# Kernel optimization log

Measured on AMD Instinct MI355X. Metric: run time of the kernel, lower is better.

## Reference

```python
import jax, jax.numpy as jnp
import numpy as np

TEMPERATURE = 0.5


def setup_inputs() -> dict:
    key = jax.random.key(0)
    k1, k2 = jax.random.split(key)
    N, D = 4096, 512
    emb_i = jax.random.normal(k1, (N, D), dtype=jnp.float32)
    emb_j = jax.random.normal(k2, (N, D), dtype=jnp.float32)
    return {"emb_i": emb_i, "emb_j": emb_j}


def reference(emb_i, emb_j):
    # L2-normalize each embedding row (F.normalize, dim=1)
    z_i = emb_i / jnp.linalg.norm(emb_i, axis=1, keepdims=True)
    z_j = emb_j / jnp.linalg.norm(emb_j, axis=1, keepdims=True)
    reps = jnp.concatenate([z_i, z_j], axis=0)  # [2N, D]
    N = emb_i.shape[0]
    M = 2 * N
    # cosine similarity of normalized vectors == dot product -> [2N, 2N]
    sim = jnp.einsum('id,jd->ij', reps, reps) / TEMPERATURE
    # denominator: sum_k!=i exp(sim[i,k]); original multiplies by one-hot complement
    exp_sim = jnp.exp(sim)
    denom = jnp.sum(exp_sim, axis=1) - jnp.diagonal(exp_sim)  # [2N]
    log_denom = jnp.log(denom)
    # positive pairs: (k, k+N) and (k+N, k)
    idx = jnp.arange(N)
    pos_ij = sim[idx, idx + N]          # sim(k, k+N)/T
    pos_ji = sim[idx + N, idx]          # sim(k+N, k)/T
    loss = jnp.sum(-(pos_ij - log_denom[:N]) - (pos_ji - log_denom[N:]))
    return loss / (2.0 * N)
```

## Files before the change

### kernel.cpp

```cpp
#include <hip/hip_runtime.h>
#include <cstdint>
#include <cstddef>

constexpr int N_ROWS = 4096;
constexpr int D      = 512;
constexpr int M      = 8192;
constexpr int NTILE  = 64;
constexpr int NBLK   = NTILE * (NTILE + 1) / 2;
constexpr int BKB    = 128;
constexpr int LDSB   = 128 * BKB;

using f32x4 = __attribute__((ext_vector_type(4))) float;
using i32x4 = __attribute__((ext_vector_type(4))) int;
using i32x8 = __attribute__((ext_vector_type(8))) int;

#define ASYNC_CP16(gsrc, ldst)                                                      \
    __builtin_amdgcn_global_load_lds(                                               \
        (const __attribute__((address_space(1))) unsigned int*)(gsrc),              \
        (__attribute__((address_space(3))) unsigned int*)(ldst), 16, 0, 0)

#define SS_FP8(pk, accum)                                                           \
    do {                                                                            \
        float f0 = __builtin_amdgcn_cvt_f32_fp8((pk), 0);                           \
        float f1 = __builtin_amdgcn_cvt_f32_fp8((pk), 1);                           \
        float f2 = __builtin_amdgcn_cvt_f32_fp8((pk), 2);                           \
        float f3 = __builtin_amdgcn_cvt_f32_fp8((pk), 3);                           \
        (accum) += f0 * f0 + f1 * f1 + f2 * f2 + f3 * f3;                           \
    } while (0)

__global__ __launch_bounds__(256) void normpos_kernel(
    const float* __restrict__ emb_i, const float* __restrict__ emb_j,
    uint8_t* __restrict__ zb, float* __restrict__ diagss,
    float* __restrict__ pos)
{
    const int wave = threadIdx.x >> 6, lane = threadIdx.x & 63;
    const int k = blockIdx.x * 4 + wave;

    const float4* a = (const float4*)(emb_i + (size_t)k * D);
    const float4* b = (const float4*)(emb_j + (size_t)k * D);
    float4 a0 = a[lane * 2], a1 = a[lane * 2 + 1];
    float4 b0 = b[lane * 2], b1 = b[lane * 2 + 1];

    float ssi = a0.x*a0.x + a0.y*a0.y + a0.z*a0.z + a0.w*a0.w
              + a1.x*a1.x + a1.y*a1.y + a1.z*a1.z + a1.w*a1.w;
    float ssj = b0.x*b0.x + b0.y*b0.y + b0.z*b0.z + b0.w*b0.w
              + b1.x*b1.x + b1.y*b1.y + b1.z*b1.z + b1.w*b1.w;
    float dp  = a0.x*b0.x + a0.y*b0.y + a0.z*b0.z + a0.w*b0.w
              + a1.x*b1.x + a1.y*b1.y + a1.z*b1.z + a1.w*b1.w;
    #pragma unroll
    for (int off = 32; off; off >>= 1) {
        ssi += __shfl_xor(ssi, off, 64);
        ssj += __shfl_xor(ssj, off, 64);
        dp  += __shfl_xor(dp,  off, 64);
    }
    const float invi = rsqrtf(ssi), invj = rsqrtf(ssj);

    const float zi[8] = {a0.x*invi, a0.y*invi, a0.z*invi, a0.w*invi,
                         a1.x*invi, a1.y*invi, a1.z*invi, a1.w*invi};
    const float zj[8] = {b0.x*invj, b0.y*invj, b0.z*invj, b0.w*invj,
                         b1.x*invj, b1.y*invj, b1.z*invj, b1.w*invj};

    int pi0 = __builtin_amdgcn_cvt_pk_fp8_f32(zi[0], zi[1], 0, false);
    pi0     = __builtin_amdgcn_cvt_pk_fp8_f32(zi[2], zi[3], pi0, true);
    int pi1 = __builtin_amdgcn_cvt_pk_fp8_f32(zi[4], zi[5], 0, false);
    pi1     = __builtin_amdgcn_cvt_pk_fp8_f32(zi[6], zi[7], pi1, true);
    int pj0 = __builtin_amdgcn_cvt_pk_fp8_f32(zj[0], zj[1], 0, false);
    pj0     = __builtin_amdgcn_cvt_pk_fp8_f32(zj[2], zj[3], pj0, true);
    int pj1 = __builtin_amdgcn_cvt_pk_fp8_f32(zj[4], zj[5], 0, false);
    pj1     = __builtin_amdgcn_cvt_pk_fp8_f32(zj[6], zj[7], pj1, true);

    float dssi = 0.f, dssj = 0.f;
    SS_FP8(pi0, dssi);
    SS_FP8(pi1, dssi);
    SS_FP8(pj0, dssj);
    SS_FP8(pj1, dssj);

    const unsigned long long vi =
        ((unsigned long long)(unsigned)pi1 << 32) | (unsigned)pi0;
    const unsigned long long vj =
        ((unsigned long long)(unsigned)pj1 << 32) | (unsigned)pj0;
    *(unsigned long long*)(zb + (size_t)k * D + lane * 8)            = vi;
    *(unsigned long long*)(zb + (size_t)(k + N_ROWS) * D + lane * 8) = vj;

    #pragma unroll
    for (int off = 32; off; off >>= 1) {
        dssi += __shfl_xor(dssi, off, 64);
        dssj += __shfl_xor(dssj, off, 64);
    }
    if (lane == 0) {
        diagss[k]          = dssi;
        diagss[k + N_ROWS] = dssj;
        pos[k]             = 2.0f * dp * invi * invj;
    }
}

__global__ __launch_bounds__(256, 2) void simgemm_kernel(
    const uint8_t* __restrict__ zb, float* __restrict__ partials)
{
    __shared__ i32x4 AsV[2 * LDSB / 16];
    __shared__ i32x4 BsV[2 * LDSB / 16];
    __shared__ float rp[4][64];
    __shared__ float cp4[4][64];
    uint8_t* As = (uint8_t*)AsV;
    uint8_t* Bs = (uint8_t*)BsV;

    const int tid  = threadIdx.x;
    const int wave = tid >> 6, lane = tid & 63;
    const int l15  = lane & 15, ks = lane >> 4;

    const int t = blockIdx.x;
    int bi = (int)((129.0f - sqrtf(129.0f * 129.0f - 8.0f * (float)t)) * 0.5f);
    while (bi > 0 && bi * (129 - bi) / 2 > t) --bi;
    while ((bi + 1) * (129 - (bi + 1)) / 2 <= t) ++bi;
    const int bj = bi + (t - bi * (129 - bi) / 2);
    const bool diag = (bi == bj);

    const int wrow = (wave >> 1) * 64, wcol = (wave & 1) * 64;

    const int srow = (lane >> 3);
    const int scol = ((lane & 7) ^ ((lane >> 3) & 7)) * 16;
    const uint8_t* gA = zb + (size_t)(bi * 128 + wave * 32 + srow) * D + scol;
    const uint8_t* gB = zb + (size_t)(bj * 128 + wave * 32 + srow) * D + scol;
    uint8_t* lA = As + wave * 32 * BKB;
    uint8_t* lB = Bs + wave * 32 * BKB;

    #pragma unroll
    for (int c = 0; c < 4; ++c) {
        ASYNC_CP16(gA + (size_t)c * 8 * D, lA + c * 8 * BKB);
        ASYNC_CP16(gB + (size_t)c * 8 * D, lB + c * 8 * BKB);
    }

    f32x4 acc[4][4] = {};

    for (int it = 0; it < D / BKB; ++it) {
        __syncthreads();

        if (it + 1 < D / BKB) {
            const int kc  = (it + 1) * BKB;
            const int off = ((it + 1) & 1) * LDSB;
            #pragma unroll
            for (int c = 0; c < 4; ++c) {
                ASYNC_CP16(gA + kc + (size_t)c * 8 * D, lA + off + c * 8 * BKB);
                ASYNC_CP16(gB + kc + (size_t)c * 8 * D, lB + off + c * 8 * BKB);
            }
        }

        const int cb = (it & 1) * LDSB;
        i32x8 af[4], bg[4];
        #pragma unroll
        for (int f = 0; f < 4; ++f) {
            {
                const int R = wrow + f * 16 + l15;
                const uint8_t* base = As + cb + R * BKB;
                const int sw = (R & 7);
                i32x4 lo = *(const i32x4*)(base + ((ks * 2)     ^ sw) * 16);
                i32x4 hi = *(const i32x4*)(base + ((ks * 2 + 1) ^ sw) * 16);
                af[f] = __builtin_shufflevector(lo, hi, 0, 1, 2, 3, 4, 5, 6, 7);
            }
            {
                const int R = wcol + f * 16 + l15;
                const uint8_t* base = Bs + cb + R * BKB;
                const int sw = (R & 7);
                i32x4 lo = *(const i32x4*)(base + ((ks * 2)     ^ sw) * 16);
                i32x4 hi = *(const i32x4*)(base + ((ks * 2 + 1) ^ sw) * 16);
                bg[f] = __builtin_shufflevector(lo, hi, 0, 1, 2, 3, 4, 5, 6, 7);
            }
        }
        #pragma unroll
        for (int i = 0; i < 4; ++i)
            #pragma unroll
            for (int j = 0; j < 4; ++j)
                acc[i][j] = __builtin_amdgcn_mfma_scale_f32_16x16x128_f8f6f4(
                    af[i], bg[j], acc[i][j], 0, 0, 0, 0x7F, 0, 0x7F);
    }

    float rowp[4][4] = {};
    #pragma unroll
    for (int j = 0; j < 4; ++j) {
        float cpj = 0.f;
        #pragma unroll
        for (int i = 0; i < 4; ++i)
            #pragma unroll
            for (int r = 0; r < 4; ++r) {
                float e = __expf(2.0f * acc[i][j][r]);
                rowp[i][r] += e;
                cpj += e;
            }
        if (!diag) {
            cpj += __shfl_xor(cpj, 16, 64);
            cpj += __shfl_xor(cpj, 32, 64);
            if (ks == 0) cp4[wave][j * 16 + l15] = cpj;
        }
    }
    #pragma unroll
    for (int i = 0; i < 4; ++i)
        #pragma unroll
        for (int r = 0; r < 4; ++r) {
            float e = rowp[i][r];
            e += __shfl_xor(e, 1, 64);
            e += __shfl_xor(e, 2, 64);
            e += __shfl_xor(e, 4, 64);
            e += __shfl_xor(e, 8, 64);
            if (l15 == 0) rp[wave][i * 16 + ks * 4 + r] = e;
        }
    __syncthreads();

    float* pA = partials + (size_t)(bi * NTILE + bj) * 128;
    float* pB = partials + (size_t)(bj * NTILE + bi) * 128;
    if (tid < 128) {
        const int h = tid >> 6, rr = tid & 63;
        pA[tid] = rp[h * 2][rr] + rp[h * 2 + 1][rr];
    } else if (!diag) {
        const int c = tid - 128, h = c >> 6, cc = c & 63;
        pB[c] = cp4[h][cc] + cp4[h + 2][cc];
    }
}

__global__ __launch_bounds__(256) void rowfin_kernel(
    const float* __restrict__ partials, const float* __restrict__ diagss,
    const float* __restrict__ pos, float* __restrict__ lgpart)
{
    const int r  = blockIdx.x;
    const int ri = threadIdx.x & 127;
    const int ch = threadIdx.x >> 7;
    const float* base = partials + (size_t)r * NTILE * 128 + ri;
    float s = 0.f;
    #pragma unroll
    for (int c = 0; c < 32; ++c)
        s += base[(size_t)(ch * 32 + c) * 128];
    __shared__ float half1[128];
    __shared__ float red[4];
    if (ch == 1) half1[ri] = s;
    __syncthreads();
    float lg = 0.f;
    if (ch == 0) {
        float rs = s + half1[ri];
        int row = r * 128 + ri;
        lg = __logf(rs - __expf(2.0f * diagss[row]));
    }
    if (threadIdx.x < 64)
        lg -= 2.0f * pos[r * 64 + threadIdx.x];
    #pragma unroll
    for (int off = 32; off; off >>= 1) lg += __shfl_xor(lg, off, 64);
    const int wave = threadIdx.x >> 6, lane = threadIdx.x & 63;
    if (lane == 0) red[wave] = lg;
    __syncthreads();
    if (threadIdx.x == 0) lgpart[r] = red[0] + red[1] + red[2] + red[3];
}

__global__ __launch_bounds__(64) void loss_kernel(
    const float* __restrict__ lgpart, float* __restrict__ out)
{
    float local = lgpart[threadIdx.x];
    #pragma unroll
    for (int off = 32; off; off >>= 1) local += __shfl_xor(local, off, 64);
    if (threadIdx.x == 0) out[0] = local * (1.0f / 8192.0f);
}

extern "C" void kernel_launch(void* const* d_in, const int* in_sizes, int n_in,
                              void* d_out, int out_size, void* d_ws, size_t ws_size,
                              hipStream_t stream)
{
    const float* emb_i = (const float*)d_in[0];
    const float* emb_j = (const float*)d_in[1];

    uint8_t* zb = (uint8_t*)d_ws;
    float* partials = (float*)((char*)d_ws + (size_t)M * D);
    float* diagss   = partials + (size_t)NTILE * NTILE * 128;
    float* pos      = diagss + M;
    float* lgpart   = pos + N_ROWS;
    float* out      = (float*)d_out;

    normpos_kernel<<<N_ROWS / 4, 256, 0, stream>>>(emb_i, emb_j, zb, diagss, pos);
    simgemm_kernel<<<NBLK, 256, 0, stream>>>(zb, partials);
    rowfin_kernel<<<NTILE, 256, 0, stream>>>(partials, diagss, pos, lgpart);
    loss_kernel<<<1, 64, 0, stream>>>(lgpart, out);
}
```

Measured before the change: 110.8 us.

## Drop LDS double buffering to single buffer and raise occupancy to four blocks

Replaces the double-buffered LDS staging with a single buffer per operand. Each K step now loads, synchronises, then computes, with an extra barrier before the next load. This halves LDS use, and launch bounds are raised to allow four blocks per CU so other blocks hide the load latency instead of in-block prefetch. It also hoists the swizzle offsets out of the fragment loop. The cost is lost intra-block overlap, an extra barrier per iteration, and tighter register limits that may cause spills.

```diff
diff --git a/kernel.cpp b/kernel.cpp
--- a/kernel.cpp
+++ b/kernel.cpp
@@ -94,11 +94,11 @@
     }
 }
 
-__global__ __launch_bounds__(256, 2) void simgemm_kernel(
+__global__ __launch_bounds__(256, 4) void simgemm_kernel(
     const uint8_t* __restrict__ zb, float* __restrict__ partials)
 {
-    __shared__ i32x4 AsV[2 * LDSB / 16];
-    __shared__ i32x4 BsV[2 * LDSB / 16];
+    __shared__ i32x4 AsV[LDSB / 16];
+    __shared__ i32x4 BsV[LDSB / 16];
     __shared__ float rp[4][64];
     __shared__ float cp4[4][64];
     uint8_t* As = (uint8_t*)AsV;
@@ -124,45 +124,34 @@
     uint8_t* lA = As + wave * 32 * BKB;
     uint8_t* lB = Bs + wave * 32 * BKB;
 
-    #pragma unroll
-    for (int c = 0; c < 4; ++c) {
-        ASYNC_CP16(gA + (size_t)c * 8 * D, lA + c * 8 * BKB);
-        ASYNC_CP16(gB + (size_t)c * 8 * D, lB + c * 8 * BKB);
-    }
-
     f32x4 acc[4][4] = {};
+    const int sw  = l15 & 7;
+    const int co0 = ((ks * 2)     ^ sw) * 16;
+    const int co1 = ((ks * 2 + 1) ^ sw) * 16;
 
     for (int it = 0; it < D / BKB; ++it) {
+        if (it > 0) __syncthreads();
+        const int kc = it * BKB;
+        #pragma unroll
+        for (int c = 0; c < 4; ++c) {
+            ASYNC_CP16(gA + kc + (size_t)c * 8 * D, lA + c * 8 * BKB);
+            ASYNC_CP16(gB + kc + (size_t)c * 8 * D, lB + c * 8 * BKB);
+        }
         __syncthreads();
 
-        if (it + 1 < D / BKB) {
-            const int kc  = (it + 1) * BKB;
-            const int off = ((it + 1) & 1) * LDSB;
-            #pragma unroll
-            for (int c = 0; c < 4; ++c) {
-                ASYNC_CP16(gA + kc + (size_t)c * 8 * D, lA + off + c * 8 * BKB);
-                ASYNC_CP16(gB + kc + (size_t)c * 8 * D, lB + off + c * 8 * BKB);
-            }
-        }
-
-        const int cb = (it & 1) * LDSB;
         i32x8 af[4], bg[4];
         #pragma unroll
         for (int f = 0; f < 4; ++f) {
             {
-                const int R = wrow + f * 16 + l15;
-                const uint8_t* base = As + cb + R * BKB;
-                const int sw = (R & 7);
-                i32x4 lo = *(const i32x4*)(base + ((ks * 2)     ^ sw) * 16);
-                i32x4 hi = *(const i32x4*)(base + ((ks * 2 + 1) ^ sw) * 16);
+                const uint8_t* base = As + (wrow + f * 16 + l15) * BKB;
+                i32x4 lo = *(const i32x4*)(base + co0);
+                i32x4 hi = *(const i32x4*)(base + co1);
                 af[f] = __builtin_shufflevector(lo, hi, 0, 1, 2, 3, 4, 5, 6, 7);
             }
             {
-                const int R = wcol + f * 16 + l15;
-                const uint8_t* base = Bs + cb + R * BKB;
-                const int sw = (R & 7);
-                i32x4 lo = *(const i32x4*)(base + ((ks * 2)     ^ sw) * 16);
-                i32x4 hi = *(const i32x4*)(base + ((ks * 2 + 1) ^ sw) * 16);
+                const uint8_t* base = Bs + (wcol + f * 16 + l15) * BKB;
+                i32x4 lo = *(const i32x4*)(base + co0);
+                i32x4 hi = *(const i32x4*)(base + co1);
                 bg[f] = __builtin_shufflevector(lo, hi, 0, 1, 2, 3, 4, 5, 6, 7);
             }
         }
```

New measurement: 119.2 us. +7.6%, slower.

## Split GEMM tile across eight waves with 32x64 per-wave subtiles

Applied to the files above, without the earlier changes.

The similarity GEMM block grows from 256 to 512 threads. Each wave now computes a 32x64 subtile instead of 64x64, which halves the accumulator registers and loads per wave. The swizzle offsets are hoisted out of the k-loop, and the row and column partial reductions are reorganised for eight waves. The goal is more waves in flight to hide LDS and MFMA latency, at the cost of more B-fragment LDS traffic per MFMA and a larger cross-wave reduction.

```diff
diff --git a/kernel.cpp b/kernel.cpp
--- a/kernel.cpp
+++ b/kernel.cpp
@@ -94,13 +94,13 @@
     }
 }
 
-__global__ __launch_bounds__(256, 2) void simgemm_kernel(
+__global__ __launch_bounds__(512, 4) void simgemm_kernel(
     const uint8_t* __restrict__ zb, float* __restrict__ partials)
 {
     __shared__ i32x4 AsV[2 * LDSB / 16];
     __shared__ i32x4 BsV[2 * LDSB / 16];
-    __shared__ float rp[4][64];
-    __shared__ float cp4[4][64];
+    __shared__ float rp[8][32];
+    __shared__ float cp8[8][64];
     uint8_t* As = (uint8_t*)AsV;
     uint8_t* Bs = (uint8_t*)BsV;
 
@@ -115,22 +115,25 @@
     const int bj = bi + (t - bi * (129 - bi) / 2);
     const bool diag = (bi == bj);
 
-    const int wrow = (wave >> 1) * 64, wcol = (wave & 1) * 64;
-
-    const int srow = (lane >> 3);
+    const int wrow = (wave >> 1) * 32;
+    const int wcol = (wave & 1) * 64;
+
     const int scol = ((lane & 7) ^ ((lane >> 3) & 7)) * 16;
-    const uint8_t* gA = zb + (size_t)(bi * 128 + wave * 32 + srow) * D + scol;
-    const uint8_t* gB = zb + (size_t)(bj * 128 + wave * 32 + srow) * D + scol;
-    uint8_t* lA = As + wave * 32 * BKB;
-    uint8_t* lB = Bs + wave * 32 * BKB;
-
-    #pragma unroll
-    for (int c = 0; c < 4; ++c) {
+    const uint8_t* gA = zb + (size_t)(bi * 128 + wave * 16 + (lane >> 3)) * D + scol;
+    const uint8_t* gB = zb + (size_t)(bj * 128 + wave * 16 + (lane >> 3)) * D + scol;
+    uint8_t* lA = As + wave * 16 * BKB;
+    uint8_t* lB = Bs + wave * 16 * BKB;
+
+    #pragma unroll
+    for (int c = 0; c < 2; ++c) {
         ASYNC_CP16(gA + (size_t)c * 8 * D, lA + c * 8 * BKB);
         ASYNC_CP16(gB + (size_t)c * 8 * D, lB + c * 8 * BKB);
     }
 
-    f32x4 acc[4][4] = {};
+    f32x4 acc[2][4] = {};
+    const int sw  = l15 & 7;
+    const int co0 = ((ks * 2)     ^ sw) * 16;
+    const int co1 = ((ks * 2 + 1) ^ sw) * 16;
 
     for (int it = 0; it < D / BKB; ++it) {
         __syncthreads();
@@ -139,47 +142,42 @@
             const int kc  = (it + 1) * BKB;
             const int off = ((it + 1) & 1) * LDSB;
             #pragma unroll
-            for (int c = 0; c < 4; ++c) {
+            for (int c = 0; c < 2; ++c) {
                 ASYNC_CP16(gA + kc + (size_t)c * 8 * D, lA + off + c * 8 * BKB);
                 ASYNC_CP16(gB + kc + (size_t)c * 8 * D, lB + off + c * 8 * BKB);
             }
         }
 
         const int cb = (it & 1) * LDSB;
-        i32x8 af[4], bg[4];
+        i32x8 af[2], bg[4];
+        #pragma unroll
+        for (int f = 0; f < 2; ++f) {
+            const uint8_t* base = As + cb + (wrow + f * 16 + l15) * BKB;
+            i32x4 lo = *(const i32x4*)(base + co0);
+            i32x4 hi = *(const i32x4*)(base + co1);
+            af[f] = __builtin_shufflevector(lo, hi, 0, 1, 2, 3, 4, 5, 6, 7);
+        }
         #pragma unroll
         for (int f = 0; f < 4; ++f) {
-            {
-                const int R = wrow + f * 16 + l15;
-                const uint8_t* base = As + cb + R * BKB;
-                const int sw = (R & 7);
-                i32x4 lo = *(const i32x4*)(base + ((ks * 2)     ^ sw) * 16);
-                i32x4 hi = *(const i32x4*)(base + ((ks * 2 + 1) ^ sw) * 16);
-                af[f] = __builtin_shufflevector(lo, hi, 0, 1, 2, 3, 4, 5, 6, 7);
-            }
-            {
-                const int R = wcol + f * 16 + l15;
-                const uint8_t* base = Bs + cb + R * BKB;
-                const int sw = (R & 7);
-                i32x4 lo = *(const i32x4*)(base + ((ks * 2)     ^ sw) * 16);
-                i32x4 hi = *(const i32x4*)(base + ((ks * 2 + 1) ^ sw) * 16);
-                bg[f] = __builtin_shufflevector(lo, hi, 0, 1, 2, 3, 4, 5, 6, 7);
-            }
-        }
-        #pragma unroll
-        for (int i = 0; i < 4; ++i)
+            const uint8_t* base = Bs + cb + (wcol + f * 16 + l15) * BKB;
+            i32x4 lo = *(const i32x4*)(base + co0);
+            i32x4 hi = *(const i32x4*)(base + co1);
+            bg[f] = __builtin_shufflevector(lo, hi, 0, 1, 2, 3, 4, 5, 6, 7);
+        }
+        #pragma unroll
+        for (int i = 0; i < 2; ++i)
             #pragma unroll
             for (int j = 0; j < 4; ++j)
                 acc[i][j] = __builtin_amdgcn_mfma_scale_f32_16x16x128_f8f6f4(
                     af[i], bg[j], acc[i][j], 0, 0, 0, 0x7F, 0, 0x7F);
     }
 
-    float rowp[4][4] = {};
+    float rowp[2][4] = {};
     #pragma unroll
     for (int j = 0; j < 4; ++j) {
         float cpj = 0.f;
         #pragma unroll
-        for (int i = 0; i < 4; ++i)
+        for (int i = 0; i < 2; ++i)
             #pragma unroll
             for (int r = 0; r < 4; ++r) {
                 float e = __expf(2.0f * acc[i][j][r]);
@@ -189,11 +187,11 @@
         if (!diag) {
             cpj += __shfl_xor(cpj, 16, 64);
             cpj += __shfl_xor(cpj, 32, 64);
-            if (ks == 0) cp4[wave][j * 16 + l15] = cpj;
-        }
-    }
-    #pragma unroll
-    for (int i = 0; i < 4; ++i)
+            if (ks == 0) cp8[wave][j * 16 + l15] = cpj;
+        }
+    }
+    #pragma unroll
+    for (int i = 0; i < 2; ++i)
         #pragma unroll
         for (int r = 0; r < 4; ++r) {
             float e = rowp[i][r];
@@ -208,11 +206,11 @@
     float* pA = partials + (size_t)(bi * NTILE + bj) * 128;
     float* pB = partials + (size_t)(bj * NTILE + bi) * 128;
     if (tid < 128) {
-        const int h = tid >> 6, rr = tid & 63;
-        pA[tid] = rp[h * 2][rr] + rp[h * 2 + 1][rr];
-    } else if (!diag) {
+        const int m = tid >> 5, rr = tid & 31;
+        pA[tid] = rp[m * 2][rr] + rp[m * 2 + 1][rr];
+    } else if (tid < 256 && !diag) {
         const int c = tid - 128, h = c >> 6, cc = c & 63;
-        pB[c] = cp4[h][cc] + cp4[h + 2][cc];
+        pB[c] = cp8[h][cc] + cp8[h + 2][cc] + cp8[h + 4][cc] + cp8[h + 6][cc];
     }
 }
 
@@ -272,7 +270,7 @@
     float* out      = (float*)d_out;
 
     normpos_kernel<<<N_ROWS / 4, 256, 0, stream>>>(emb_i, emb_j, zb, diagss, pos);
-    simgemm_kernel<<<NBLK, 256, 0, stream>>>(zb, partials);
+    simgemm_kernel<<<NBLK, 512, 0, stream>>>(zb, partials);
     rowfin_kernel<<<NTILE, 256, 0, stream>>>(partials, diagss, pos, lgpart);
     loss_kernel<<<1, 64, 0, stream>>>(lgpart, out);
 }
```

New measurement: 106.8 us. 1.04x faster.
